# Optimization experiments

Hardware: AMD Instinct MI355X
Metric: run time of the kernel (lower is better)

The kernel has to match this reference:

```python
import jax, jax.numpy as jnp
import numpy as np

M = 262144      # total tokens
K = 64          # n_channels (input dim)
N = 64          # expert_size (output dim)
E = 8           # n_experts


def setup_inputs() -> dict:
    key = jax.random.key(0)
    k1, k2, k3 = jax.random.split(key, 3)
    x = jax.random.normal(k1, (M, K), dtype=jnp.float32)
    sel = jax.random.randint(k2, (M,), 0, E, dtype=jnp.int32)
    w = jax.random.normal(k3, (E, K, N), dtype=jnp.float32)
    return {"x": x, "sel": sel, "w": w}


def reference(x, sel, w):
    # cvmm: out[m] = x[m] @ w[sel[m]]  (per-token expert GEMM)
    # Loop over the small fixed expert set; accumulate masked dense GEMMs
    # instead of materializing w[sel] ([M,K,N], which would be huge).
    E_ = w.shape[0]
    out = jnp.zeros((x.shape[0], w.shape[2]), dtype=x.dtype)
    for e in range(E_):
        mask = (sel == e)[:, None]           # [M,1]
        out = out + jnp.where(mask, x @ w[e], jnp.zeros((), x.dtype))
    return out
```

## Files before the change

### kernel.cpp

```cpp
#include <hip/hip_runtime.h>


typedef __bf16 bf16x8 __attribute__((ext_vector_type(8)));
typedef __bf16 bf16x4 __attribute__((ext_vector_type(4)));
typedef float  floatx4 __attribute__((ext_vector_type(4)));

#define NCHUNK 4
#define CT 128
#define BLK_TOK (NCHUNK * CT)

__global__ __launch_bounds__(256) void wpack_kernel(
    const float* __restrict__ w, bf16x8* __restrict__ wp)
{
    const int id   = blockIdx.x * 256 + threadIdx.x;
    const int lane = id & 63;
    const int nt   = (id >> 6) & 3;
    const int t    = (id >> 8) & 1;
    const int e    = id >> 9;
    const int q = lane >> 4, l16 = lane & 15;
    const float* src = w + (((e * 64) + t * 32 + q * 8) * 64) + nt * 16 + l16;
    bf16x8 f;
#pragma unroll
    for (int j = 0; j < 8; ++j) f[j] = (__bf16)src[j * 64];
    wp[id] = f;
}

#define BAR() do {                                         \
    __builtin_amdgcn_sched_barrier(0);                     \
    asm volatile("s_waitcnt lgkmcnt(0)" ::: "memory");     \
    __builtin_amdgcn_s_barrier();                          \
    __builtin_amdgcn_sched_barrier(0);                     \
} while (0)

__global__ __launch_bounds__(256, 2) void cvmm_kernel(
    const float* __restrict__ x,
    const int* __restrict__ sel,
    const bf16x8* __restrict__ wp,
    float* __restrict__ out)
{
    __shared__ __align__(16) unsigned char xls[2][16384];
    __shared__ unsigned int sortLds[2][128];
    __shared__ unsigned int invLds[2][128];

    const int T    = threadIdx.x;
    const int lane = T & 63;
    const int wv   = T >> 6;
    const int q    = lane >> 4;
    const int l16  = lane & 15;
    const int n0   = wv << 4;

    const int wrow = T >> 4;
    const int gl   = (T & 15) >> 1;
    const int half = (T & 1) * 8;
    const int roffA = ((q)     ^ (l16 & 7)) << 4;
    const int roffB = ((q + 4) ^ (l16 & 7)) << 4;

    const long base = (long)blockIdx.x * BLK_TOK;

    bf16x8 zf;
#pragma unroll
    for (int j = 0; j < 8; ++j) zf[j] = (__bf16)0.0f;

    const bf16x8* wpw = wp + wv * 64 + lane;

    int sA0 = 0, sA1 = 0, sB0 = 0, sB1 = 0;
    if (wv == 0) {
        const int* sp = sel + base;
        sA0 = sp[lane];      sA1 = sp[64 + lane];
        sB0 = sp[CT + lane]; sB1 = sp[CT + 64 + lane];
    }
    floatx4 RA[8], RB[8];
    {
        const float* xc = x + base * 64;
#pragma unroll
        for (int i = 0; i < 8; ++i)
            RA[i] = *(const floatx4*)(xc + i * 1024 + 4 * T);
#pragma unroll
        for (int i = 0; i < 8; ++i)
            RB[i] = *(const floatx4*)(xc + CT * 64 + i * 1024 + 4 * T);
    }

#define CHUNK_BODY(c, RX, sX0, sX1)                                          \
    {                                                                        \
        const int buf = (c) & 1;                                             \
                          \
        if (wv == 0) {                                                       \
            const unsigned long long lt = (1ull << lane) - 1;                \
            int slot0 = 0, slot1 = 0, pref = 0;                              \
            _Pragma("unroll")                                                \
            for (int e = 0; e < 8; ++e) {                                    \
                unsigned long long m0 = __ballot(sX0 == e);                  \
                unsigned long long m1 = __ballot(sX1 == e);                  \
                if (sX0 == e) slot0 = pref + __popcll(m0 & lt);              \
                if (sX1 == e) slot1 = pref + __popcll(m0) + __popcll(m1 & lt);\
                pref += __popcll(m0) + __popcll(m1);                         \
            }                                                                \
            invLds[buf][lane]      = (unsigned)slot0;                        \
            invLds[buf][64 + lane] = (unsigned)slot1;                        \
            sortLds[buf][slot0] = (unsigned)lane        | ((unsigned)sX0 << 8); \
            sortLds[buf][slot1] = (unsigned)(64 + lane) | ((unsigned)sX1 << 8); \
        }                                                                    \
        BAR();                                                               \
              \
        {                                                                    \
            unsigned char* lb = xls[buf];                                    \
            _Pragma("unroll")                                                \
            for (int i = 0; i < 8; ++i) {                                    \
                const int slot = (int)invLds[buf][i * 16 + wrow];            \
                bf16x4 v;                                                    \
                v[0] = (__bf16)RX[i][0]; v[1] = (__bf16)RX[i][1];            \
                v[2] = (__bf16)RX[i][2]; v[3] = (__bf16)RX[i][3];            \
                *(bf16x4*)(lb + slot * 128 + ((gl ^ (slot & 7)) << 4) + half) = v; \
            }                                                                \
        }                                                                    \
         \
        if (wv == 0 && (c) + 2 < NCHUNK) {                                   \
            const int* sp = sel + base + ((c) + 2) * CT;                     \
            sX0 = sp[lane]; sX1 = sp[64 + lane];                             \
        }                                                                    \
        BAR();                                                               \
                      \
        if ((c) + 2 < NCHUNK) {                                              \
            const float* xc = x + (base + ((c) + 2) * CT) * 64;              \
            _Pragma("unroll")                                                \
            for (int i = 0; i < 8; ++i)                                      \
                RX[i] = *(const floatx4*)(xc + i * 1024 + 4 * T);            \
        }                                                                    \
                        \
        {                                                                    \
            const unsigned char* lb = xls[buf];                              \
            const long ct0 = base + (c) * CT;                                \
            _Pragma("unroll")                                                \
            for (int i = 0; i < 8; ++i) {                                    \
                const unsigned u = sortLds[buf][i * 16 + l16];               \
                const int tokL = (int)(u & 255u);                            \
                const int el   = (int)(u >> 8);                              \
                const int rb2  = (i * 16 + l16) * 128;                       \
                const bf16x8 af0 = *(const bf16x8*)(lb + rb2 + roffA);       \
                const bf16x8 af1 = *(const bf16x8*)(lb + rb2 + roffB);       \
                const int elo = __builtin_amdgcn_readfirstlane(el);          \
                const int ehi = __builtin_amdgcn_readlane(el, 15);           \
                floatx4 acc = {0.0f, 0.0f, 0.0f, 0.0f};                      \
                if (elo == ehi) {                                            \
                    acc = __builtin_amdgcn_mfma_f32_16x16x32_bf16(           \
                              wpw[elo * 512],       af0, acc, 0, 0, 0);      \
                    acc = __builtin_amdgcn_mfma_f32_16x16x32_bf16(           \
                              wpw[elo * 512 + 256], af1, acc, 0, 0, 0);      \
                } else {                                                     \
                    for (int e = elo; e <= ehi; ++e) {                       \
                        const bool ok = (el == e);                           \
                        acc = __builtin_amdgcn_mfma_f32_16x16x32_bf16(       \
                                  wpw[e * 512],       ok ? af0 : zf, acc, 0, 0, 0); \
                        acc = __builtin_amdgcn_mfma_f32_16x16x32_bf16(       \
                                  wpw[e * 512 + 256], ok ? af1 : zf, acc, 0, 0, 0); \
                    }                                                        \
                }                                                            \
                float* op = out + (ct0 + tokL) * 64 + n0 + (q << 2);         \
                *(floatx4*)op = acc;                                         \
            }                                                                \
        }                                                                    \
    }

    CHUNK_BODY(0, RA, sA0, sA1)
    CHUNK_BODY(1, RB, sB0, sB1)
    CHUNK_BODY(2, RA, sA0, sA1)
    CHUNK_BODY(3, RB, sB0, sB1)
#undef CHUNK_BODY
}

extern "C" void kernel_launch(void* const* d_in, const int* in_sizes, int n_in,
                              void* d_out, int out_size, void* d_ws, size_t ws_size,
                              hipStream_t stream) {
    const float* x   = (const float*)d_in[0];
    const int*   sel = (const int*)d_in[1];
    const float* w   = (const float*)d_in[2];
    float*       out = (float*)d_out;

    const int M = in_sizes[0] / 64;
    bf16x8* wp = (bf16x8*)d_ws;

    wpack_kernel<<<16, 256, 0, stream>>>(w, wp);
    cvmm_kernel<<<M / BLK_TOK, 256, 0, stream>>>(x, sel, wp, out);
}
```

Baseline: 125.8 us.

## Stage outputs in LDS for coalesced stores, keep expert weights in registers, interleave chunks

Output rows are now written to a padded LDS buffer in token order and streamed to global memory as fully coalesced 16-byte stores one iteration later, replacing scattered per-token stores. All eight experts' packed weight fragments are loaded once into registers rather than re-read from global for each MFMA. Chunks are assigned strided across a fixed grid of 512 blocks, and the next chunk's loads are issued before the previous output is streamed. This raises register and LDS use, which may lower occupancy, and hardcodes the grid size to the problem's M.

```diff
diff --git a/kernel.cpp b/kernel.cpp
--- a/kernel.cpp
+++ b/kernel.cpp
@@ -5,9 +5,9 @@
 typedef __bf16 bf16x4 __attribute__((ext_vector_type(4)));
 typedef float  floatx4 __attribute__((ext_vector_type(4)));
 
-#define NCHUNK 4
-#define CT 128
-#define BLK_TOK (NCHUNK * CT)
+#define CT    128
+#define NBLK  512
+#define ITERS 4
 
 __global__ __launch_bounds__(256) void wpack_kernel(
     const float* __restrict__ w, bf16x8* __restrict__ wp)
@@ -38,52 +38,76 @@
     const bf16x8* __restrict__ wp,
     float* __restrict__ out)
 {
-    __shared__ __align__(16) unsigned char xls[2][16384];
-    __shared__ unsigned int sortLds[2][128];
-    __shared__ unsigned int invLds[2][128];
+    __shared__ __align__(16) unsigned char xls[2][CT * 128];
+    __shared__ __align__(16) unsigned char obuf[CT * 272];
+    __shared__ unsigned int sortLds[2][CT];
+    __shared__ unsigned int invLds[2][CT];
 
     const int T    = threadIdx.x;
     const int lane = T & 63;
     const int wv   = T >> 6;
     const int q    = lane >> 4;
     const int l16  = lane & 15;
-    const int n0   = wv << 4;
 
     const int wrow = T >> 4;
     const int gl   = (T & 15) >> 1;
-    const int half = (T & 1) * 8;
+    const int hB   = (T & 1) * 8;
     const int roffA = ((q)     ^ (l16 & 7)) << 4;
     const int roffB = ((q + 4) ^ (l16 & 7)) << 4;
 
-    const long base = (long)blockIdx.x * BLK_TOK;
-
     bf16x8 zf;
 #pragma unroll
     for (int j = 0; j < 8; ++j) zf[j] = (__bf16)0.0f;
 
     const bf16x8* wpw = wp + wv * 64 + lane;
+    floatx4 bfp[8][2];
+#pragma unroll
+    for (int e = 0; e < 8; ++e)
+#pragma unroll
+        for (int t = 0; t < 2; ++t)
+            bfp[e][t] = __builtin_bit_cast(floatx4, wpw[e * 512 + t * 256]);
+#pragma unroll
+    for (int e = 0; e < 8; ++e)
+        asm volatile("" : "+v"(bfp[e][0]), "+v"(bfp[e][1]));
 
     int sA0 = 0, sA1 = 0, sB0 = 0, sB1 = 0;
-    if (wv == 0) {
-        const int* sp = sel + base;
-        sA0 = sp[lane];      sA1 = sp[64 + lane];
-        sB0 = sp[CT + lane]; sB1 = sp[CT + 64 + lane];
-    }
     floatx4 RA[8], RB[8];
     {
-        const float* xc = x + base * 64;
+        const long i0 = (long)blockIdx.x;
+        const long i1 = (long)NBLK + blockIdx.x;
+        if (wv == 0) {
+            sA0 = sel[i0 * CT + lane]; sA1 = sel[i0 * CT + 64 + lane];
+            sB0 = sel[i1 * CT + lane]; sB1 = sel[i1 * CT + 64 + lane];
+        }
+        const float* xc0 = x + i0 * CT * 64;
+        const float* xc1 = x + i1 * CT * 64;
+        __builtin_amdgcn_sched_barrier(0);
 #pragma unroll
         for (int i = 0; i < 8; ++i)
-            RA[i] = *(const floatx4*)(xc + i * 1024 + 4 * T);
+            RA[i] = *(const floatx4*)(xc0 + i * 1024 + 4 * T);
 #pragma unroll
         for (int i = 0; i < 8; ++i)
-            RB[i] = *(const floatx4*)(xc + CT * 64 + i * 1024 + 4 * T);
+            RB[i] = *(const floatx4*)(xc1 + i * 1024 + 4 * T);
+        __builtin_amdgcn_sched_barrier(0);
     }
 
-#define CHUNK_BODY(c, RX, sX0, sX1)                                          \
+#define STREAM(pg)                                                           \
     {                                                                        \
-        const int buf = (c) & 1;                                             \
-                          \
+        float* og = out + ((long)(pg) * NBLK + blockIdx.x) * CT * 64;        \
+        _Pragma("unroll")                                                    \
+        for (int i = 0; i < 8; ++i) {                                        \
+            const int G = i * 256 + T;                                       \
+            const floatx4 v =                                                \
+                *(const floatx4*)(obuf + (G >> 4) * 272 + (G & 15) * 16);    \
+            *(floatx4*)(og + (long)G * 4) = v;                               \
+        }                                                                    \
+    }
+
+#define BODY(g, RX, sX0, sX1)                                                \
+    {                                                                        \
+        const int  buf  = (g) & 1;                                           \
+        const long item = (long)(g) * NBLK + blockIdx.x;                     \
+                         \
         if (wv == 0) {                                                       \
             const unsigned long long lt = (1ull << lane) - 1;                \
             int slot0 = 0, slot1 = 0, pref = 0;                              \
@@ -92,7 +116,7 @@
                 unsigned long long m0 = __ballot(sX0 == e);                  \
                 unsigned long long m1 = __ballot(sX1 == e);                  \
                 if (sX0 == e) slot0 = pref + __popcll(m0 & lt);              \
-                if (sX1 == e) slot1 = pref + __popcll(m0) + __popcll(m1 & lt);\
+                if (sX1 == e) slot1 = pref + __popcll(m0) + __popcll(m1 & lt); \
                 pref += __popcll(m0) + __popcll(m1);                         \
             }                                                                \
             invLds[buf][lane]      = (unsigned)slot0;                        \
@@ -101,7 +125,7 @@
             sortLds[buf][slot1] = (unsigned)(64 + lane) | ((unsigned)sX1 << 8); \
         }                                                                    \
         BAR();                                                               \
-              \
+          \
         {                                                                    \
             unsigned char* lb = xls[buf];                                    \
             _Pragma("unroll")                                                \
@@ -110,62 +134,66 @@
                 bf16x4 v;                                                    \
                 v[0] = (__bf16)RX[i][0]; v[1] = (__bf16)RX[i][1];            \
                 v[2] = (__bf16)RX[i][2]; v[3] = (__bf16)RX[i][3];            \
-                *(bf16x4*)(lb + slot * 128 + ((gl ^ (slot & 7)) << 4) + half) = v; \
-            }                                                                \
-        }                                                                    \
-         \
-        if (wv == 0 && (c) + 2 < NCHUNK) {                                   \
-            const int* sp = sel + base + ((c) + 2) * CT;                     \
-            sX0 = sp[lane]; sX1 = sp[64 + lane];                             \
-        }                                                                    \
-        BAR();                                                               \
-                      \
-        if ((c) + 2 < NCHUNK) {                                              \
-            const float* xc = x + (base + ((c) + 2) * CT) * 64;              \
+                *(bf16x4*)(lb + slot * 128 + ((gl ^ (slot & 7)) << 4) + hB) = v; \
+            }                                                                \
+        }                                                                    \
+             \
+        if ((g) + 2 < ITERS) {                                               \
+            const long ni = (long)((g) + 2) * NBLK + blockIdx.x;             \
+            if (wv == 0) {                                                   \
+                sX0 = sel[ni * CT + lane];                                   \
+                sX1 = sel[ni * CT + 64 + lane];                              \
+            }                                                                \
+            const float* xc = x + ni * CT * 64;                              \
+            __builtin_amdgcn_sched_barrier(0);                               \
             _Pragma("unroll")                                                \
             for (int i = 0; i < 8; ++i)                                      \
                 RX[i] = *(const floatx4*)(xc + i * 1024 + 4 * T);            \
-        }                                                                    \
-                        \
+            __builtin_amdgcn_sched_barrier(0);                               \
+        }                                                                    \
+           \
+        if ((g) > 0) STREAM((g) - 1);                                        \
+        BAR();                                                               \
+                                    \
         {                                                                    \
             const unsigned char* lb = xls[buf];                              \
-            const long ct0 = base + (c) * CT;                                \
             _Pragma("unroll")                                                \
             for (int i = 0; i < 8; ++i) {                                    \
                 const unsigned u = sortLds[buf][i * 16 + l16];               \
                 const int tokL = (int)(u & 255u);                            \
                 const int el   = (int)(u >> 8);                              \
-                const int rb2  = (i * 16 + l16) * 128;                       \
-                const bf16x8 af0 = *(const bf16x8*)(lb + rb2 + roffA);       \
-                const bf16x8 af1 = *(const bf16x8*)(lb + rb2 + roffB);       \
+                const int rb   = (i * 16 + l16) * 128;                       \
+                const bf16x8 af0 = *(const bf16x8*)(lb + rb + roffA);        \
+                const bf16x8 af1 = *(const bf16x8*)(lb + rb + roffB);        \
                 const int elo = __builtin_amdgcn_readfirstlane(el);          \
                 const int ehi = __builtin_amdgcn_readlane(el, 15);           \
                 floatx4 acc = {0.0f, 0.0f, 0.0f, 0.0f};                      \
-                if (elo == ehi) {                                            \
-                    acc = __builtin_amdgcn_mfma_f32_16x16x32_bf16(           \
-                              wpw[elo * 512],       af0, acc, 0, 0, 0);      \
-                    acc = __builtin_amdgcn_mfma_f32_16x16x32_bf16(           \
-                              wpw[elo * 512 + 256], af1, acc, 0, 0, 0);      \
-                } else {                                                     \
-                    for (int e = elo; e <= ehi; ++e) {                       \
+                _Pragma("unroll")                                            \
+                for (int e = 0; e < 8; ++e) {                                \
+                    if (e >= elo && e <= ehi) {                              \
                         const bool ok = (el == e);                           \
                         acc = __builtin_amdgcn_mfma_f32_16x16x32_bf16(       \
-                                  wpw[e * 512],       ok ? af0 : zf, acc, 0, 0, 0); \
+                                  __builtin_bit_cast(bf16x8, bfp[e][0]),     \
+                                  ok ? af0 : zf, acc, 0, 0, 0);              \
                         acc = __builtin_amdgcn_mfma_f32_16x16x32_bf16(       \
-                                  wpw[e * 512 + 256], ok ? af1 : zf, acc, 0, 0, 0); \
+                                  __builtin_bit_cast(bf16x8, bfp[e][1]),     \
+                                  ok ? af1 : zf, acc, 0, 0, 0);              \
                     }                                                        \
                 }                                                            \
-                float* op = out + (ct0 + tokL) * 64 + n0 + (q << 2);         \
-                *(floatx4*)op = acc;                                         \
+                *(floatx4*)(obuf + tokL * 272 + (wv * 4 + q) * 16) = acc;    \
             }                                                                \
         }                                                                    \
     }
 
-    CHUNK_BODY(0, RA, sA0, sA1)
-    CHUNK_BODY(1, RB, sB0, sB1)
-    CHUNK_BODY(2, RA, sA0, sA1)
-    CHUNK_BODY(3, RB, sB0, sB1)
-#undef CHUNK_BODY
+    BODY(0, RA, sA0, sA1)
+    BODY(1, RB, sB0, sB1)
+    BODY(2, RA, sA0, sA1)
+    BODY(3, RB, sB0, sB1)
+#undef BODY
+
+    BAR();
+    STREAM(ITERS - 1);
+#undef STREAM
 }
 
 extern "C" void kernel_launch(void* const* d_in, const int* in_sizes, int n_in,
@@ -176,9 +204,8 @@
     const float* w   = (const float*)d_in[2];
     float*       out = (float*)d_out;
 
-    const int M = in_sizes[0] / 64;
     bf16x8* wp = (bf16x8*)d_ws;
 
     wpack_kernel<<<16, 256, 0, stream>>>(w, wp);
-    cvmm_kernel<<<M / BLK_TOK, 256, 0, stream>>>(x, sel, wp, out);
+    cvmm_kernel<<<NBLK, 256, 0, stream>>>(x, sel, wp, out);
 }
```

New measurement: 121.8 us. 1.03x faster.
